# Optimization experiments

Measured on AMD Instinct MI355X. Metric: run time of the kernel, lower is better.

## Reference

```python
import jax, jax.numpy as jnp
import numpy as np

N = 4096      # batch_size
D = 256       # projection dim
TEMP = 0.5    # temperature


def setup_inputs() -> dict:
    key = jax.random.key(0)
    k1, k2 = jax.random.split(key)
    return {
        "emb_i": jax.random.normal(k1, (N, D), dtype=jnp.float32),
        "emb_j": jax.random.normal(k2, (N, D), dtype=jnp.float32),
    }


def reference(emb_i, emb_j):
    # L2-normalize rows (F.normalize, dim=1)
    z_i = emb_i / jnp.maximum(jnp.linalg.norm(emb_i, axis=1, keepdims=True), 1e-12)
    z_j = emb_j / jnp.maximum(jnp.linalg.norm(emb_j, axis=1, keepdims=True), 1e-12)
    rep = jnp.concatenate([z_i, z_j], axis=0)            # [2N, D]

    # cosine similarity of unit vectors == dot product -> GEMM instead of O(N^2 D) broadcast
    sim = rep @ rep.T                                    # [2N, 2N]

    # positives: diag(sim, +N) and diag(sim, -N) are both sum(z_i*z_j, axis=1)
    pos_ij = jnp.sum(z_i * z_j, axis=1)                  # [N]
    positives = jnp.concatenate([pos_ij, pos_ij], axis=0)  # [2N]

    # mask keeps exactly the two cross-view blocks (main diagonal lies in same-view blocks)
    idx = jnp.arange(2 * N)
    mask = (idx[:, None] < N) != (idx[None, :] < N)      # [2N, 2N] bool

    nominator = jnp.exp(positives / TEMP)                # [2N]
    denominator = jnp.sum(jnp.where(mask, jnp.exp(sim / TEMP), 0.0), axis=1)  # [2N]

    loss_partial = -jnp.log(nominator / (0.5 * denominator))
    return jnp.sum(loss_partial) / (2 * N)
```

## Files before the change

kernel.cpp:

```cpp
#include <hip/hip_runtime.h>
#include <math.h>

#define NROWS 4096
#define DDIM  256
#define BM 128
#define BN 128
#define LOG2E2 2.8853900817779268f

typedef __attribute__((ext_vector_type(8))) short short8;
typedef __attribute__((ext_vector_type(4))) float f32x4;

__device__ __forceinline__ unsigned short f2bf(float f) {
    unsigned int u = __float_as_uint(f);
    u += 0x7fffu + ((u >> 16) & 1u);
    return (unsigned short)(u >> 16);
}

__device__ __forceinline__ float exp2_fast(float x) {
#if __has_builtin(__builtin_amdgcn_exp2f)
    return __builtin_amdgcn_exp2f(x);
#else
    return exp2f(x);
#endif
}

#define GLOAD_LDS16(gsrc, ldst)                                          \
    __builtin_amdgcn_global_load_lds(                                    \
        (__attribute__((address_space(1))) void*)(gsrc),                 \
        (__attribute__((address_space(3))) void*)(ldst), 16, 0, 0)

__global__ __launch_bounds__(256) void normalize_kernel(
    const float* __restrict__ emb_i, const float* __restrict__ emb_j,
    unsigned short* __restrict__ zi, unsigned short* __restrict__ zj,
    float* __restrict__ pos, float* __restrict__ sums )
{
    if (threadIdx.x < 8) sums[blockIdx.x * 8 + threadIdx.x] = 0.0f;

    const int wave = threadIdx.x >> 6;
    const int lane = threadIdx.x & 63;
    const int row  = blockIdx.x * 4 + wave;

    const float4 vi = *((const float4*)(emb_i + (size_t)row * DDIM) + lane);
    const float4 vj = *((const float4*)(emb_j + (size_t)row * DDIM) + lane);

    float ssi = vi.x*vi.x + vi.y*vi.y + vi.z*vi.z + vi.w*vi.w;
    float ssj = vj.x*vj.x + vj.y*vj.y + vj.z*vj.z + vj.w*vj.w;
    #pragma unroll
    for (int m = 1; m < 64; m <<= 1) {
        ssi += __shfl_xor(ssi, m);
        ssj += __shfl_xor(ssj, m);
    }
    const float ri = 1.0f / fmaxf(sqrtf(ssi), 1e-12f);
    const float rj = 1.0f / fmaxf(sqrtf(ssj), 1e-12f);

    const float zix = vi.x*ri, ziy = vi.y*ri, ziz = vi.z*ri, ziw = vi.w*ri;
    const float zjx = vj.x*rj, zjy = vj.y*rj, zjz = vj.z*rj, zjw = vj.w*rj;

    float p = zix*zjx + ziy*zjy + ziz*zjz + ziw*zjw;
    #pragma unroll
    for (int m = 1; m < 64; m <<= 1) p += __shfl_xor(p, m);
    if (lane == 0) pos[row] = p;

    ushort4 oi = { f2bf(zix*LOG2E2), f2bf(ziy*LOG2E2), f2bf(ziz*LOG2E2), f2bf(ziw*LOG2E2) };
    ushort4 oj = { f2bf(zjx), f2bf(zjy), f2bf(zjz), f2bf(zjw) };
    *((ushort4*)(zi + (size_t)row * DDIM) + lane) = oi;
    *((ushort4*)(zj + (size_t)row * DDIM) + lane) = oj;
}

__global__ __launch_bounds__(256) void gemm_fused_kernel(
    const unsigned short* __restrict__ zi, const unsigned short* __restrict__ zj,
    float* __restrict__ rowsum, float* __restrict__ colsum)
{
    __shared__ unsigned short As[BM * DDIM];
    __shared__ unsigned short Bs[BN * DDIM];

    const int tid  = threadIdx.x;
    const int lane = tid & 63;
    const int wave = tid >> 6;
    const int g    = lane >> 4;
    const int fr   = lane & 15;
    const int wr   = wave >> 1;
    const int wc   = wave & 1;
    const int bm   = blockIdx.x * BM;
    const int bn   = blockIdx.y * BN;

    f32x4 acc[4][4] = {};

    #pragma unroll
    for (int it = 0; it < 16; ++it) {
        const int L    = it * 256 + tid;
        const int row  = L >> 5;
        const int sl   = L & 31;
        const int soff = ((sl ^ (row & 7)) << 3);
        const int lb   = (it * 256 + wave * 64) << 3;
        GLOAD_LDS16(zi + (size_t)(bm + row) * DDIM + soff, As + lb);
        GLOAD_LDS16(zj + (size_t)(bn + row) * DDIM + soff, Bs + lb);
    }
    __syncthreads();

    #pragma unroll
    for (int kk = 0; kk < 8; ++kk) {
        const int cs = kk * 4 + g;
        short8 a[4], b[4];
        #pragma unroll
        for (int mi = 0; mi < 4; ++mi) {
            const int row = wr * 64 + mi * 16 + fr;
            a[mi] = *(const short8*)&As[row * DDIM + ((cs ^ (fr & 7)) << 3)];
        }
        #pragma unroll
        for (int ni = 0; ni < 4; ++ni) {
            const int row = wc * 64 + ni * 16 + fr;
            b[ni] = *(const short8*)&Bs[row * DDIM + ((cs ^ (fr & 7)) << 3)];
        }
        #pragma unroll
        for (int mi = 0; mi < 4; ++mi)
            #pragma unroll
            for (int ni = 0; ni < 4; ++ni)
                acc[mi][ni] = __builtin_amdgcn_mfma_f32_16x16x32_bf16(
                    a[mi], b[ni], acc[mi][ni], 0, 0, 0);
    }

    float rp[4][4];
    float cp[4] = {0.f, 0.f, 0.f, 0.f};
    #pragma unroll
    for (int mi = 0; mi < 4; ++mi)
        #pragma unroll
        for (int j = 0; j < 4; ++j) rp[mi][j] = 0.f;

    #pragma unroll
    for (int mi = 0; mi < 4; ++mi)
        #pragma unroll
        for (int ni = 0; ni < 4; ++ni)
            #pragma unroll
            for (int j = 0; j < 4; ++j) {
                const float e = exp2_fast(acc[mi][ni][j]);
                rp[mi][j] += e;
                cp[ni]    += e;
            }

    #pragma unroll
    for (int mi = 0; mi < 4; ++mi)
        #pragma unroll
        for (int j = 0; j < 4; ++j) {
            float v = rp[mi][j];
            v += __shfl_xor(v, 1); v += __shfl_xor(v, 2);
            v += __shfl_xor(v, 4); v += __shfl_xor(v, 8);
            if (fr == 0)
                atomicAdd(&rowsum[bm + wr * 64 + mi * 16 + g * 4 + j], v);
        }

    #pragma unroll
    for (int ni = 0; ni < 4; ++ni) {
        float v = cp[ni];
        v += __shfl_xor(v, 16); v += __shfl_xor(v, 32);
        if (g == 0)
            atomicAdd(&colsum[bn + wc * 64 + ni * 16 + fr], v);
    }
}

__global__ __launch_bounds__(512) void finalize_kernel(
    const float* __restrict__ pos, const float* __restrict__ rowsum,
    const float* __restrict__ colsum, float* __restrict__ out)
{
    float s = 0.0f;
    for (int r = threadIdx.x; r < NROWS; r += 512) {
        s += -4.0f * pos[r] + logf(0.25f * rowsum[r] * colsum[r]);
    }
    __shared__ float part[8];
    #pragma unroll
    for (int m = 1; m < 64; m <<= 1) s += __shfl_xor(s, m);
    if ((threadIdx.x & 63) == 0) part[threadIdx.x >> 6] = s;
    __syncthreads();
    if (threadIdx.x == 0) {
        float t = 0.f;
        #pragma unroll
        for (int w = 0; w < 8; ++w) t += part[w];
        out[0] = t / (2.0f * NROWS);
    }
}

extern "C" void kernel_launch(void* const* d_in, const int* in_sizes, int n_in,
                              void* d_out, int out_size, void* d_ws, size_t ws_size,
                              hipStream_t stream)
{
    const float* emb_i = (const float*)d_in[0];
    const float* emb_j = (const float*)d_in[1];

    unsigned short* zi = (unsigned short*)d_ws;
    unsigned short* zj = zi + (size_t)NROWS * DDIM;
    float* pos    = (float*)(zj + (size_t)NROWS * DDIM);
    float* rowsum = pos + NROWS;
    float* colsum = rowsum + NROWS;

    normalize_kernel<<<NROWS / 4, 256, 0, stream>>>(emb_i, emb_j, zi, zj, pos, rowsum);

    dim3 grid(NROWS / BM, NROWS / BN);
    gemm_fused_kernel<<<grid, 256, 0, stream>>>(zi, zj, rowsum, colsum);

    finalize_kernel<<<1, 512, 0, stream>>>(pos, rowsum, colsum, (float*)d_out);
}
```

Before: 93.26 us.

## Use 128x256 output tiles with K-chunked LDS staging in fused GEMM

Widens the GEMM block tile from 128x128 to 128x256 so each wave computes a 64x128 sub-tile. The full-K LDS preload (128 KB) is replaced by a loop over four K chunks of 64, cutting LDS to 48 KB and allowing two blocks per CU. This raises reuse per loaded A fragment and halves the number of column blocks and rowsum atomics. The cost is more accumulator registers per thread (128 floats) and a synchronous load-then-compute loop with no double buffering.

```diff
diff --git a/kernel.cpp b/kernel.cpp
--- a/kernel.cpp
+++ b/kernel.cpp
@@ -4,7 +4,8 @@
 #define NROWS 4096
 #define DDIM  256
 #define BM 128
-#define BN 128
+#define BN 256
+#define BK 64
 #define LOG2E2 2.8853900817779268f
 
 typedef __attribute__((ext_vector_type(8))) short short8;
@@ -67,12 +68,12 @@
     *((ushort4*)(zj + (size_t)row * DDIM) + lane) = oj;
 }
 
-__global__ __launch_bounds__(256) void gemm_fused_kernel(
+__global__ __launch_bounds__(256, 2) void gemm_fused_kernel(
     const unsigned short* __restrict__ zi, const unsigned short* __restrict__ zj,
     float* __restrict__ rowsum, float* __restrict__ colsum)
 {
-    __shared__ unsigned short As[BM * DDIM];
-    __shared__ unsigned short Bs[BN * DDIM];
+    __shared__ unsigned short As[BM * BK];
+    __shared__ unsigned short Bs[BN * BK];
 
     const int tid  = threadIdx.x;
     const int lane = tid & 63;
@@ -84,44 +85,48 @@
     const int bm   = blockIdx.x * BM;
     const int bn   = blockIdx.y * BN;
 
-    f32x4 acc[4][4] = {};
-
-    #pragma unroll
-    for (int it = 0; it < 16; ++it) {
-        const int L    = it * 256 + tid;
-        const int row  = L >> 5;
-        const int sl   = L & 31;
-        const int soff = ((sl ^ (row & 7)) << 3);
-        const int lb   = (it * 256 + wave * 64) << 3;
-        GLOAD_LDS16(zi + (size_t)(bm + row) * DDIM + soff, As + lb);
-        GLOAD_LDS16(zj + (size_t)(bn + row) * DDIM + soff, Bs + lb);
-    }
-    __syncthreads();
-
-    #pragma unroll
-    for (int kk = 0; kk < 8; ++kk) {
-        const int cs = kk * 4 + g;
-        short8 a[4], b[4];
-        #pragma unroll
-        for (int mi = 0; mi < 4; ++mi) {
-            const int row = wr * 64 + mi * 16 + fr;
-            a[mi] = *(const short8*)&As[row * DDIM + ((cs ^ (fr & 7)) << 3)];
-        }
-        #pragma unroll
-        for (int ni = 0; ni < 4; ++ni) {
-            const int row = wc * 64 + ni * 16 + fr;
-            b[ni] = *(const short8*)&Bs[row * DDIM + ((cs ^ (fr & 7)) << 3)];
-        }
-        #pragma unroll
-        for (int mi = 0; mi < 4; ++mi)
-            #pragma unroll
-            for (int ni = 0; ni < 4; ++ni)
-                acc[mi][ni] = __builtin_amdgcn_mfma_f32_16x16x32_bf16(
-                    a[mi], b[ni], acc[mi][ni], 0, 0, 0);
+    f32x4 acc[4][8] = {};
+
+    const int srow = tid >> 3;
+    const int soff = (((tid & 7) ^ (srow & 7)) << 3);
+
+    for (int k0 = 0; k0 < DDIM; k0 += BK) {
+        #pragma unroll
+        for (int it = 0; it < 4; ++it) {
+            const int row = it * 32 + srow;
+            const int lb  = (it * 256 + wave * 64) << 3;
+            GLOAD_LDS16(zi + (size_t)(bm + row) * DDIM + k0 + soff, As + lb);
+        }
+        #pragma unroll
+        for (int it = 0; it < 8; ++it) {
+            const int row = it * 32 + srow;
+            const int lb  = (it * 256 + wave * 64) << 3;
+            GLOAD_LDS16(zj + (size_t)(bn + row) * DDIM + k0 + soff, Bs + lb);
+        }
+        __syncthreads();
+
+        #pragma unroll
+        for (int kk = 0; kk < 2; ++kk) {
+            const int coff = (((kk * 4 + g) ^ (fr & 7)) << 3);
+            short8 a[4], b[8];
+            #pragma unroll
+            for (int mi = 0; mi < 4; ++mi)
+                a[mi] = *(const short8*)&As[(wr * 64 + mi * 16 + fr) * BK + coff];
+            #pragma unroll
+            for (int ni = 0; ni < 8; ++ni)
+                b[ni] = *(const short8*)&Bs[(wc * 128 + ni * 16 + fr) * BK + coff];
+            #pragma unroll
+            for (int mi = 0; mi < 4; ++mi)
+                #pragma unroll
+                for (int ni = 0; ni < 8; ++ni)
+                    acc[mi][ni] = __builtin_amdgcn_mfma_f32_16x16x32_bf16(
+                        a[mi], b[ni], acc[mi][ni], 0, 0, 0);
+        }
+        __syncthreads();
     }
 
     float rp[4][4];
-    float cp[4] = {0.f, 0.f, 0.f, 0.f};
+    float cp[8] = {0.f,0.f,0.f,0.f,0.f,0.f,0.f,0.f};
     #pragma unroll
     for (int mi = 0; mi < 4; ++mi)
         #pragma unroll
@@ -130,7 +135,7 @@
     #pragma unroll
     for (int mi = 0; mi < 4; ++mi)
         #pragma unroll
-        for (int ni = 0; ni < 4; ++ni)
+        for (int ni = 0; ni < 8; ++ni)
             #pragma unroll
             for (int j = 0; j < 4; ++j) {
                 const float e = exp2_fast(acc[mi][ni][j]);
@@ -150,11 +155,11 @@
         }
 
     #pragma unroll
-    for (int ni = 0; ni < 4; ++ni) {
+    for (int ni = 0; ni < 8; ++ni) {
         float v = cp[ni];
         v += __shfl_xor(v, 16); v += __shfl_xor(v, 32);
         if (g == 0)
-            atomicAdd(&colsum[bn + wc * 64 + ni * 16 + fr], v);
+            atomicAdd(&colsum[bn + wc * 128 + ni * 16 + fr], v);
     }
 }
 
```

Result: faster. 77.35 us (-17.1%).
